# Performance work log

Measured on AMD Instinct MI355X. Metric: run time of the kernel, lower is better.

## Reference

```python
import jax, jax.numpy as jnp
import numpy as np

N = 471
TOPK = 50
T = 16384
M = 128


def setup_inputs() -> dict:
    key = jax.random.key(0)
    ks = jax.random.split(key, 6)
    x = jax.random.normal(ks[0], (T, N), dtype=jnp.float32)
    q_t = jax.random.normal(ks[1], (M, N), dtype=jnp.float32)
    # parameters, initialized as in the torch module
    w = 0.0021 + 0.0005 * jax.random.normal(ks[2], (N,), dtype=jnp.float32)
    b1 = jax.random.normal(ks[3], (N,), dtype=jnp.float32)  # unused in forward math
    alpha = jnp.array([10.0], dtype=jnp.float32)
    lamda = jnp.array([0.1], dtype=jnp.float32)
    rho = jnp.array([0.001], dtype=jnp.float32)
    mu = jnp.array([0.001], dtype=jnp.float32)
    bound = 1.0 / np.sqrt(N)
    linear_w = jax.random.uniform(ks[4], (N, N), minval=-bound, maxval=bound, dtype=jnp.float32)
    linear_b = jax.random.uniform(ks[5], (N,), minval=-bound, maxval=bound, dtype=jnp.float32)
    return {"x": x, "q_t": q_t, "w": w, "b1": b1, "alpha": alpha,
            "lamda": lamda, "rho": rho, "mu": mu,
            "linear_w": linear_w, "linear_b": linear_b}


def reference(x, q_t, w, b1, alpha, lamda, rho, mu, linear_w, linear_b):
    # W2 = mean over time of Linear(x); identical every unrolled iteration -> compute once
    W2 = (x @ linear_w.T + linear_b).mean(axis=0)           # [N]
    pinvQ = jnp.linalg.pinv(q_t @ q_t.T)                    # [M,M], identical every iter

    def theta_update(z, u):
        v = u - rho * (z - w)                               # [N]
        return alpha * (pinvQ @ (q_t @ v))                  # [M]

    def z_update(z, u, theta):
        b = w + (q_t.T @ theta) / N                         # [N]
        grad_z = W2 + rho * (z - b) + u
        grad_z = grad_z + 2.0 * lamda * (jnp.sum(z) - 1.0)  # scalar * ones broadcast
        grad_z = grad_z + 2.0 * lamda * jnp.minimum(0.0, z)
        z_new = jax.nn.relu(z - mu * grad_z)
        _, idx = jax.lax.top_k(z_new, TOPK)
        mask = jnp.zeros_like(z_new).at[idx].set(1.0)
        return z_new * mask

    z = jnp.zeros(N, dtype=x.dtype)
    u = jnp.zeros(N, dtype=x.dtype)
    for _ in range(9):
        theta = theta_update(z, u)
        z = z_update(z, u, theta)
        b = w + (q_t.T @ theta) / N
        u = u + rho * (z - b)
    theta = theta_update(z, u)
    z = z_update(z, u, theta)
    return z / (jnp.sum(z) + 1e-8)
```

## Files before the change

kernel.cpp:

```cpp
#include <hip/hip_runtime.h>

#define NDIM 471
#define MD   128
#define TD   16384
#define KSEL 50
#define CGIT 4

#define WS_PART   0
#define WS_G      120832
#define WS_T1     137216
#define WS_XBAR   197888
#define WS_W2     198400
#define WS_RW     198912
#define WS_CTR    199384
#define WS_R      199424

static __device__ __forceinline__ float rdl(float v, int lane){
    return __int_as_float(__builtin_amdgcn_readlane(__float_as_int(v), lane));
}

__global__ __launch_bounds__(512) void k_gram_colsum(const float* __restrict__ qt,
                                                     const float* __restrict__ x,
                                                     const float* __restrict__ wv,
                                                     float* __restrict__ ws){
    int lane = threadIdx.x & 63, wid = threadIdx.x >> 6;
    if (blockIdx.x < 256){
        float* G = ws + WS_G;
        int gw = blockIdx.x * 8 + wid;
        int i = gw >> 4, jb = gw & 15;
        float qi[8];
#pragma unroll
        for (int s = 0; s < 8; ++s){ int idx = lane + 64*s; qi[s] = (idx < NDIM) ? qt[i*NDIM + idx] : 0.f; }
#pragma unroll
        for (int t = 0; t < 8; ++t){
            int j = jb + 16*t;
            float acc = 0.f;
#pragma unroll
            for (int s = 0; s < 8; ++s){
                int idx = lane + 64*s;
                float qj = (idx < NDIM) ? qt[j*NDIM + idx] : 0.f;
                acc = fmaf(qi[s], qj, acc);
            }
#pragma unroll
            for (int d = 1; d < 64; d <<= 1) acc += __shfl_xor(acc, d);
            if (lane == 0) G[i*MD + j] = acc;
        }
    } else {
        int cb = blockIdx.x - 256;
        int col = threadIdx.x;
        if (col < NDIM){
            const float* xp = x + (size_t)cb*64*NDIM + col;
            float acc = 0.f;
#pragma unroll 4
            for (int r = 0; r < 64; ++r) acc += xp[(size_t)r*NDIM];
            ws[WS_PART + cb*NDIM + col] = acc;
        }
        if (cb < 16){
            int m = cb*8 + wid;
            float acc = 0.f;
#pragma unroll
            for (int s = 0; s < 8; ++s){
                int idx = lane + 64*s;
                if (idx < NDIM) acc = fmaf(qt[m*NDIM + idx], wv[idx], acc);
            }
#pragma unroll
            for (int d = 1; d < 64; d <<= 1) acc += __shfl_xor(acc, d);
            if (lane == 0) ws[WS_T1 + m] = acc;
        }
    }
}

#define G_LD(n) float4 t##n = *(const float4*)(Gp + 4*(n)); \
                float Ga##n = t##n.x, Gb##n = t##n.y, Gc##n = t##n.z, Gd##n = t##n.w;
#define G_DOT(n) pa = fmaf(Ga##n, rdl(rch.x, 2*(n)),   pa); \
                 pb = fmaf(Gb##n, rdl(rch.y, 2*(n)),   pb); \
                 pa = fmaf(Gc##n, rdl(rch.x, 2*(n)+1), pa); \
                 pb = fmaf(Gd##n, rdl(rch.y, 2*(n)+1), pb);

__global__ __launch_bounds__(256, 1) void k_cg_xbar(const float* __restrict__ qt,
                                                    const float* __restrict__ alpha,
                                                    float* __restrict__ ws){
    int tid = threadIdx.x, lane = tid & 63, wid = tid >> 6;
    if (blockIdx.x == 130 && tid == 0)
        __hip_atomic_store((unsigned*)(ws + WS_CTR), 0u, __ATOMIC_RELEASE, __HIP_MEMORY_SCOPE_AGENT);
    __shared__ __align__(16) float rl[2][128];
    __shared__ float part[2][2][128];
    __shared__ float red2[4][2];
    {
        int row = tid & 127, seg = tid >> 7;
        int c   = seg;
        int col = blockIdx.x*2 + c;
        const float* Gp = ws + WS_G + row*MD + seg*64;
        G_LD(0) G_LD(1) G_LD(2)  G_LD(3)  G_LD(4)  G_LD(5)  G_LD(6)  G_LD(7)
        G_LD(8) G_LD(9) G_LD(10) G_LD(11) G_LD(12) G_LD(13) G_LD(14) G_LD(15)
        float bvv = (col < NDIM) ? qt[row*NDIM + col] : ws[WS_T1 + row];
        float xv = 0.f, rv = bvv, pv = 0.f, sv = 0.f, gam = 1.f, alf = 1.f;
        rl[c][row] = rv;
        for (int it = 0; it < CGIT; ++it){
            __syncthreads();
#pragma unroll
            for (int cc = 0; cc < 2; ++cc){
                float2 rch = *(const float2*)&rl[cc][seg*64 + 2*(lane & 31)];
                float pa = 0.f, pb = 0.f;
                G_DOT(0) G_DOT(1) G_DOT(2)  G_DOT(3)  G_DOT(4)  G_DOT(5)  G_DOT(6)  G_DOT(7)
                G_DOT(8) G_DOT(9) G_DOT(10) G_DOT(11) G_DOT(12) G_DOT(13) G_DOT(14) G_DOT(15)
                part[seg][cc][row] = pa + pb;
            }
            __syncthreads();
            float y = part[0][c][row] + part[1][c][row];
            float t0 = rv*rv, t1 = y*rv;
#pragma unroll
            for (int d = 1; d < 64; d <<= 1){ t0 += __shfl_xor(t0, d); t1 += __shfl_xor(t1, d); }
            if (lane == 0){ red2[wid][0] = t0; red2[wid][1] = t1; }
            __syncthreads();
            float gp = red2[2*c][0] + red2[2*c+1][0];
            float dl = red2[2*c][1] + red2[2*c+1][1];
            float bet, anew;
            if (it == 0){ bet = 0.f; anew = gp / fmaxf(dl, 1e-30f); }
            else { bet = gp / fmaxf(gam, 1e-30f); anew = gp / fmaxf(dl - bet*gp/alf, 1e-30f); }
            pv = fmaf(bet, pv, rv);
            sv = fmaf(bet, sv, y);
            xv = fmaf(anew, pv, xv);
            rv = fmaf(-anew, sv, rv);
            gam = gp; alf = anew;
            rl[c][row] = rv;
        }
        rl[c][row] = xv;
        __syncthreads();
        float sc = alpha[0] / (float)NDIM;
        float2 wc0 = ((const float2*)&rl[0][0])[lane];
        float2 wc1 = ((const float2*)&rl[1][0])[lane];
        int i0 = tid;
        int i1 = (tid + 256 < NDIM) ? tid + 256 : (NDIM - 1);
        float a0=0.f, a1=0.f, b0=0.f, b1=0.f;
#pragma unroll
        for (int l = 0; l < 64; ++l){
            float w0a = rdl(wc0.x, l), w0b = rdl(wc0.y, l);
            float w1a = rdl(wc1.x, l), w1b = rdl(wc1.y, l);
            float qa0 = qt[(2*l+0)*NDIM + i0], qa1 = qt[(2*l+0)*NDIM + i1];
            float qb0 = qt[(2*l+1)*NDIM + i0], qb1 = qt[(2*l+1)*NDIM + i1];
            a0 = fmaf(qa0, w0a, a0); a0 = fmaf(qb0, w0b, a0);
            a1 = fmaf(qa1, w0a, a1); a1 = fmaf(qb1, w0b, a1);
            b0 = fmaf(qa0, w1a, b0); b0 = fmaf(qb0, w1b, b0);
            b1 = fmaf(qa1, w1a, b1); b1 = fmaf(qb1, w1b, b1);
        }
        int col0 = blockIdx.x*2, col1 = col0 + 1;
        ws[WS_R + (size_t)col0*NDIM + i0] = sc*a0;
        if (tid + 256 < NDIM) ws[WS_R + (size_t)col0*NDIM + tid+256] = sc*a1;
        if (col1 < NDIM){
            ws[WS_R + (size_t)col1*NDIM + i0] = sc*b0;
            if (tid + 256 < NDIM) ws[WS_R + (size_t)col1*NDIM + tid+256] = sc*b1;
        } else {
            ws[WS_RW + i0] = sc*b0;
            if (tid + 256 < NDIM) ws[WS_RW + tid+256] = sc*b1;
        }
    }
    if (blockIdx.x < 59){
        __shared__ float p2[4][8];
        __syncthreads();
        int b2 = blockIdx.x;
        int cl = tid & 7, seg2 = tid >> 3;
        int col = b2*8 + cl;
        float acc = 0.f;
        if (col < NDIM){
#pragma unroll
            for (int q = 0; q < 8; ++q) acc += ws[WS_PART + (seg2*8 + q)*NDIM + col];
        }
        acc += __shfl_xor(acc, 8);
        acc += __shfl_xor(acc, 16);
        acc += __shfl_xor(acc, 32);
        if (lane < 8) p2[wid][lane] = acc;
        __syncthreads();
        if (tid < 8){
            float t = ((p2[0][tid] + p2[1][tid]) + (p2[2][tid] + p2[3][tid]));
            int c2 = b2*8 + tid;
            if (c2 < NDIM) ws[WS_XBAR + c2] = t * (1.0f / TD);
        }
    }
}

__global__ __launch_bounds__(512, 2) void k_w2_iter(const float* __restrict__ lw, const float* __restrict__ lb,
                                              const float* __restrict__ wv,
                                              const float* __restrict__ alpha, const float* __restrict__ lamda,
                                              const float* __restrict__ rho_p, const float* __restrict__ mu_p,
                                              float* __restrict__ ws, float* __restrict__ out){
    int tid = threadIdx.x, lane = tid & 63, wid = tid >> 6;
    unsigned* ctr = (unsigned*)(ws + WS_CTR);

    if (blockIdx.x < 59){
        int i = blockIdx.x*8 + wid;
        if (i < NDIM){
            float acc = 0.f;
#pragma unroll
            for (int s = 0; s < 8; ++s){
                int idx = lane + 64*s;
                if (idx < NDIM) acc = fmaf(lw[(size_t)i*NDIM + idx], ws[WS_XBAR + idx], acc);
            }
#pragma unroll
            for (int d = 1; d < 64; d <<= 1) acc += __shfl_xor(acc, d);
            if (lane == 0) ws[WS_W2 + i] = acc + lb[i];
        }
        __syncthreads();
        if (tid == 0){
            __threadfence();
            __hip_atomic_fetch_add(ctr, 1u, __ATOMIC_RELEASE, __HIP_MEMORY_SCOPE_AGENT);
        }
        return;
    }

    bool act = tid < NDIM;
    int ti = act ? tid : 0;
    float rho = rho_p[0], mu = mu_p[0], lam = lamda[0];
    float sc  = alpha[0] / (float)NDIM;
    float wi  = act ? wv[tid]         : 0.f;
    float Rwi = act ? ws[WS_RW + tid] : 0.f;

    __shared__ __align__(16) unsigned bins[1024];
    __shared__ __align__(8) float2 spair[64];
    __shared__ float warr[8];
    __shared__ unsigned wcnt[8];

    bins[tid] = 0u; bins[tid + 512] = 0u;
    if (tid == 0){
        while (__hip_atomic_load(ctr, __ATOMIC_ACQUIRE, __HIP_MEMORY_SCOPE_AGENT) < 59u)
            __builtin_amdgcn_s_sleep(8);
    }
    __syncthreads();
    float W2i = act ? ws[WS_W2 + tid] : 0.f;

    float z = 0.f, u = 0.f, Ruv = 0.f, Rzv = 0.f, Sz = 0.f;
    for (int it = 0; it < 10; ++it){
        float Rv = Ruv - rho*(Rzv - Rwi);
        float b  = wi + Rv;
        float grad = W2i + rho*(z - b) + u + 2.f*lam*(Sz - 1.f);
        float zn = z - mu*grad;
        zn = (act && zn > 0.f) ? zn : 0.f;
        unsigned bits = __float_as_uint(zn);

        unsigned prefix = 0, need = KSEL;
#pragma unroll
        for (int pass = 3; pass >= 0; --pass){
            int sh = pass*8;
            unsigned* bp = bins + ((3 - pass) << 8);
            bool av = (pass == 3) || ((bits >> (sh + 8)) == (prefix >> (sh + 8)));
            if (av) atomicAdd(&bp[(bits >> sh) & 255u], 1u);
            __syncthreads();
            int base = 255 - 4*lane;
            uint4 bq = *(const uint4*)&bp[base - 3];
            unsigned b3 = bq.x, b2 = bq.y, b1 = bq.z, b0 = bq.w;
            unsigned csum = b0 + b1 + b2 + b3;
            unsigned incl = csum;
#pragma unroll
            for (int d = 1; d < 64; d <<= 1){ unsigned t = __shfl_up(incl, d); if (lane >= d) incl += t; }
            unsigned excl = incl - csum;
            bool hit = (excl < need) && (need <= incl);
            unsigned long long hm = __ballot(hit);
            int hl = __ffsll((long long)hm) - 1;
            unsigned c0 = excl + b0, c1 = c0 + b1, c2 = c1 + b2;
            int byte; unsigned above, cntc;
            if      (need <= c0){ byte = base;   above = excl; cntc = b0; }
            else if (need <= c1){ byte = base-1; above = c0;   cntc = b1; }
            else if (need <= c2){ byte = base-2; above = c1;   cntc = b2; }
            else                { byte = base-3; above = c2;   cntc = b3; }
            byte  = __shfl(byte, hl);
            above = (unsigned)__shfl((int)above, hl);
            cntc  = (unsigned)__shfl((int)cntc, hl);
            prefix |= ((unsigned)byte) << sh;
            need -= above;
            if (cntc == need) break;
        }
        z = (act && bits >= prefix) ? zn : 0.f;

        bool flag = z > 0.f;
        unsigned long long mb = __ballot(flag);
        float v = z;
#pragma unroll
        for (int d = 1; d < 64; d <<= 1) v += __shfl_xor(v, d);
        if (lane == 0){ warr[wid] = v; wcnt[wid] = (unsigned)__popcll(mb); }
        __syncthreads();
        Sz = ((warr[0]+warr[1])+(warr[2]+warr[3])) + ((warr[4]+warr[5])+(warr[6]+warr[7]));

        if (it < 9){
            unsigned off = 0;
#pragma unroll
            for (int w2 = 0; w2 < 8; ++w2) if (w2 < wid) off += wcnt[w2];
            off += (unsigned)__popcll(mb & ((1ull << lane) - 1ull));
            int cnt = 0;
#pragma unroll
            for (int w2 = 0; w2 < 8; ++w2) cnt += (int)wcnt[w2];
            if (flag){ spair[off] = make_float2(__int_as_float(tid), z); }
            if (tid >= cnt && tid < 64){ spair[tid] = make_float2(__int_as_float(0), 0.f); }
            bins[tid] = 0u; bins[tid + 512] = 0u;
            __syncthreads();

            float2 pp = spair[lane];
            const float* Rb = ws + WS_R;
            float rvv[56];
#pragma unroll
            for (int s = 0; s < 56; ++s){
                int j = __float_as_int(rdl(pp.x, s));
                rvv[s] = Rb[(size_t)j*NDIM + ti];
            }
            float a0=0.f, a1=0.f, a2=0.f, a3=0.f;
#pragma unroll
            for (int s = 0; s < 56; s += 4){
                a0 = fmaf(rvv[s+0], rdl(pp.y, s+0), a0);
                a1 = fmaf(rvv[s+1], rdl(pp.y, s+1), a1);
                a2 = fmaf(rvv[s+2], rdl(pp.y, s+2), a2);
                a3 = fmaf(rvv[s+3], rdl(pp.y, s+3), a3);
            }
            float acc = (a0+a1) + (a2+a3);
            float Rbv = Rwi + sc*Rv;
            u   += rho*(z - b);
            Ruv += rho*(acc - Rbv);
            Rzv  = acc;
        }
    }
    if (act) out[tid] = z / (Sz + 1e-8f);
}

extern "C" void kernel_launch(void* const* d_in, const int* in_sizes, int n_in,
                              void* d_out, int out_size, void* d_ws, size_t ws_size,
                              hipStream_t stream) {
    const float* x     = (const float*)d_in[0];
    const float* qt    = (const float*)d_in[1];
    const float* wv    = (const float*)d_in[2];
    const float* alpha = (const float*)d_in[4];
    const float* lamda = (const float*)d_in[5];
    const float* rho   = (const float*)d_in[6];
    const float* mu    = (const float*)d_in[7];
    const float* lw    = (const float*)d_in[8];
    const float* lb    = (const float*)d_in[9];
    float* out = (float*)d_out;
    float* ws  = (float*)d_ws;

    k_gram_colsum<<<512, 512, 0, stream>>>(qt, x, wv, ws);
    k_cg_xbar    <<<236, 256, 0, stream>>>(qt, alpha, ws);
    k_w2_iter    <<<60,  512, 0, stream>>>(lw, lb, wv, alpha, lamda, rho, mu, ws, out);
}
```

Before: 60.55 us.

## Fuse three kernels into one persistent kernel with atomic-counter dataflow sync

Merges the Gram/colsum, CG solve, and W2/iteration kernels into a single 256-block launch. Stages are ordered by per-stage atomic counters with release/acquire spin-waits instead of kernel boundaries, and a memset resets the counters. Each block now does the Gram work, then part of the x column sum, then either a CG column pair, an xbar/W2 slice, or the final iteration loop. The aim is to remove launch gaps and to overlap independent stages, at the cost of spin-wait overhead and relying on all 256 blocks being co-resident.

After: 124.1 us. 105% more time.

```diff
diff --git a/kernel.cpp b/kernel.cpp
--- a/kernel.cpp
+++ b/kernel.cpp
@@ -19,14 +19,45 @@
     return __int_as_float(__builtin_amdgcn_readlane(__float_as_int(v), lane));
 }
 
-__global__ __launch_bounds__(512) void k_gram_colsum(const float* __restrict__ qt,
-                                                     const float* __restrict__ x,
-                                                     const float* __restrict__ wv,
-                                                     float* __restrict__ ws){
-    int lane = threadIdx.x & 63, wid = threadIdx.x >> 6;
-    if (blockIdx.x < 256){
+static __device__ __forceinline__ void rel_add(unsigned* c){
+    if (threadIdx.x == 0){
+        __threadfence();
+        __hip_atomic_fetch_add(c, 1u, __ATOMIC_RELEASE, __HIP_MEMORY_SCOPE_AGENT);
+    }
+}
+static __device__ __forceinline__ void acq_wait(unsigned* c, unsigned tgt){
+    if (threadIdx.x == 0){
+        while (__hip_atomic_load(c, __ATOMIC_ACQUIRE, __HIP_MEMORY_SCOPE_AGENT) < tgt)
+            __builtin_amdgcn_s_sleep(2);
+    }
+    __syncthreads();
+}
+
+#define G_LDm(n) float4 t##n = cgact ? *(const float4*)(Gp + 4*(n)) : f4z; \
+                 float Ga##n = t##n.x, Gb##n = t##n.y, Gc##n = t##n.z, Gd##n = t##n.w;
+#define G_DOT(n) pa = fmaf(Ga##n, rdl(rch.x, 2*(n)),   pa); \
+                 pb = fmaf(Gb##n, rdl(rch.y, 2*(n)),   pb); \
+                 pa = fmaf(Gc##n, rdl(rch.x, 2*(n)+1), pa); \
+                 pb = fmaf(Gd##n, rdl(rch.y, 2*(n)+1), pb);
+
+__global__ __launch_bounds__(512) void k_mega(const float* __restrict__ qt,
+                                              const float* __restrict__ x,
+                                              const float* __restrict__ wv,
+                                              const float* __restrict__ alpha,
+                                              const float* __restrict__ lamda,
+                                              const float* __restrict__ rho_p,
+                                              const float* __restrict__ mu_p,
+                                              const float* __restrict__ lw,
+                                              const float* __restrict__ lb,
+                                              float* __restrict__ ws,
+                                              float* __restrict__ out){
+    int tid = threadIdx.x, lane = tid & 63, wid = tid >> 6;
+    int b = blockIdx.x;
+    unsigned* C = (unsigned*)(ws + WS_CTR);
+
+    {
         float* G = ws + WS_G;
-        int gw = blockIdx.x * 8 + wid;
+        int gw = b*8 + wid;
         int i = gw >> 4, jb = gw & 15;
         float qi[8];
 #pragma unroll
@@ -45,18 +76,8 @@
             for (int d = 1; d < 64; d <<= 1) acc += __shfl_xor(acc, d);
             if (lane == 0) G[i*MD + j] = acc;
         }
-    } else {
-        int cb = blockIdx.x - 256;
-        int col = threadIdx.x;
-        if (col < NDIM){
-            const float* xp = x + (size_t)cb*64*NDIM + col;
-            float acc = 0.f;
-#pragma unroll 4
-            for (int r = 0; r < 64; ++r) acc += xp[(size_t)r*NDIM];
-            ws[WS_PART + cb*NDIM + col] = acc;
-        }
-        if (cb < 16){
-            int m = cb*8 + wid;
+        if (b < 16){
+            int m = b*8 + wid;
             float acc = 0.f;
 #pragma unroll
             for (int s = 0; s < 8; ++s){
@@ -67,129 +88,131 @@
             for (int d = 1; d < 64; d <<= 1) acc += __shfl_xor(acc, d);
             if (lane == 0) ws[WS_T1 + m] = acc;
         }
-    }
-}
-
-#define G_LD(n) float4 t##n = *(const float4*)(Gp + 4*(n)); \
-                float Ga##n = t##n.x, Gb##n = t##n.y, Gc##n = t##n.z, Gd##n = t##n.w;
-#define G_DOT(n) pa = fmaf(Ga##n, rdl(rch.x, 2*(n)),   pa); \
-                 pb = fmaf(Gb##n, rdl(rch.y, 2*(n)),   pb); \
-                 pa = fmaf(Gc##n, rdl(rch.x, 2*(n)+1), pa); \
-                 pb = fmaf(Gd##n, rdl(rch.y, 2*(n)+1), pb);
-
-__global__ __launch_bounds__(256, 1) void k_cg_xbar(const float* __restrict__ qt,
-                                                    const float* __restrict__ alpha,
-                                                    float* __restrict__ ws){
-    int tid = threadIdx.x, lane = tid & 63, wid = tid >> 6;
-    if (blockIdx.x == 130 && tid == 0)
-        __hip_atomic_store((unsigned*)(ws + WS_CTR), 0u, __ATOMIC_RELEASE, __HIP_MEMORY_SCOPE_AGENT);
-    __shared__ __align__(16) float rl[2][128];
-    __shared__ float part[2][2][128];
-    __shared__ float red2[4][2];
+        __syncthreads();
+        if (tid == 0){
+            __threadfence();
+            __hip_atomic_fetch_add(&C[0], 1u, __ATOMIC_RELEASE, __HIP_MEMORY_SCOPE_AGENT);
+            if (b < 16) __hip_atomic_fetch_add(&C[1], 1u, __ATOMIC_RELEASE, __HIP_MEMORY_SCOPE_AGENT);
+        }
+    }
+
     {
-        int row = tid & 127, seg = tid >> 7;
+        int col = tid;
+        if (col < NDIM){
+            const float* xp = x + (size_t)b*64*NDIM + col;
+            float acc = 0.f;
+#pragma unroll 4
+            for (int r = 0; r < 64; ++r) acc += xp[(size_t)r*NDIM];
+            ws[WS_PART + b*NDIM + col] = acc;
+        }
+        __syncthreads();
+        rel_add(&C[2]);
+    }
+
+    if (b < 236){
+        __shared__ __align__(16) float rl[2][128];
+        __shared__ float part[2][2][128];
+        __shared__ float red2[4][2];
+        acq_wait(&C[0], 256);
+        acq_wait(&C[1], 16);
+        bool cgact = tid < 256;
+        float4 f4z = make_float4(0.f,0.f,0.f,0.f);
+        int row = tid & 127, seg = (tid >> 7) & 1;
         int c   = seg;
-        int col = blockIdx.x*2 + c;
+        int col = b*2 + c;
         const float* Gp = ws + WS_G + row*MD + seg*64;
-        G_LD(0) G_LD(1) G_LD(2)  G_LD(3)  G_LD(4)  G_LD(5)  G_LD(6)  G_LD(7)
-        G_LD(8) G_LD(9) G_LD(10) G_LD(11) G_LD(12) G_LD(13) G_LD(14) G_LD(15)
-        float bvv = (col < NDIM) ? qt[row*NDIM + col] : ws[WS_T1 + row];
+        G_LDm(0) G_LDm(1) G_LDm(2)  G_LDm(3)  G_LDm(4)  G_LDm(5)  G_LDm(6)  G_LDm(7)
+        G_LDm(8) G_LDm(9) G_LDm(10) G_LDm(11) G_LDm(12) G_LDm(13) G_LDm(14) G_LDm(15)
+        float bvv = cgact ? ((col < NDIM) ? qt[row*NDIM + col] : ws[WS_T1 + row]) : 0.f;
         float xv = 0.f, rv = bvv, pv = 0.f, sv = 0.f, gam = 1.f, alf = 1.f;
-        rl[c][row] = rv;
+        if (cgact) rl[c][row] = rv;
         for (int it = 0; it < CGIT; ++it){
             __syncthreads();
-#pragma unroll
-            for (int cc = 0; cc < 2; ++cc){
-                float2 rch = *(const float2*)&rl[cc][seg*64 + 2*(lane & 31)];
-                float pa = 0.f, pb = 0.f;
-                G_DOT(0) G_DOT(1) G_DOT(2)  G_DOT(3)  G_DOT(4)  G_DOT(5)  G_DOT(6)  G_DOT(7)
-                G_DOT(8) G_DOT(9) G_DOT(10) G_DOT(11) G_DOT(12) G_DOT(13) G_DOT(14) G_DOT(15)
-                part[seg][cc][row] = pa + pb;
+            if (cgact){
+#pragma unroll
+                for (int cc = 0; cc < 2; ++cc){
+                    float2 rch = *(const float2*)&rl[cc][seg*64 + 2*(lane & 31)];
+                    float pa = 0.f, pb = 0.f;
+                    G_DOT(0) G_DOT(1) G_DOT(2)  G_DOT(3)  G_DOT(4)  G_DOT(5)  G_DOT(6)  G_DOT(7)
+                    G_DOT(8) G_DOT(9) G_DOT(10) G_DOT(11) G_DOT(12) G_DOT(13) G_DOT(14) G_DOT(15)
+                    part[seg][cc][row] = pa + pb;
+                }
             }
             __syncthreads();
-            float y = part[0][c][row] + part[1][c][row];
-            float t0 = rv*rv, t1 = y*rv;
-#pragma unroll
-            for (int d = 1; d < 64; d <<= 1){ t0 += __shfl_xor(t0, d); t1 += __shfl_xor(t1, d); }
-            if (lane == 0){ red2[wid][0] = t0; red2[wid][1] = t1; }
+            float y = 0.f, t0 = 0.f, t1 = 0.f;
+            if (cgact){
+                y = part[0][c][row] + part[1][c][row];
+                t0 = rv*rv; t1 = y*rv;
+#pragma unroll
+                for (int d = 1; d < 64; d <<= 1){ t0 += __shfl_xor(t0, d); t1 += __shfl_xor(t1, d); }
+                if (lane == 0){ red2[wid][0] = t0; red2[wid][1] = t1; }
+            }
             __syncthreads();
-            float gp = red2[2*c][0] + red2[2*c+1][0];
-            float dl = red2[2*c][1] + red2[2*c+1][1];
-            float bet, anew;
-            if (it == 0){ bet = 0.f; anew = gp / fmaxf(dl, 1e-30f); }
-            else { bet = gp / fmaxf(gam, 1e-30f); anew = gp / fmaxf(dl - bet*gp/alf, 1e-30f); }
-            pv = fmaf(bet, pv, rv);
-            sv = fmaf(bet, sv, y);
-            xv = fmaf(anew, pv, xv);
-            rv = fmaf(-anew, sv, rv);
-            gam = gp; alf = anew;
-            rl[c][row] = rv;
-        }
-        rl[c][row] = xv;
-        __syncthreads();
-        float sc = alpha[0] / (float)NDIM;
-        float2 wc0 = ((const float2*)&rl[0][0])[lane];
-        float2 wc1 = ((const float2*)&rl[1][0])[lane];
-        int i0 = tid;
-        int i1 = (tid + 256 < NDIM) ? tid + 256 : (NDIM - 1);
-        float a0=0.f, a1=0.f, b0=0.f, b1=0.f;
-#pragma unroll
-        for (int l = 0; l < 64; ++l){
-            float w0a = rdl(wc0.x, l), w0b = rdl(wc0.y, l);
-            float w1a = rdl(wc1.x, l), w1b = rdl(wc1.y, l);
-            float qa0 = qt[(2*l+0)*NDIM + i0], qa1 = qt[(2*l+0)*NDIM + i1];
-            float qb0 = qt[(2*l+1)*NDIM + i0], qb1 = qt[(2*l+1)*NDIM + i1];
-            a0 = fmaf(qa0, w0a, a0); a0 = fmaf(qb0, w0b, a0);
-            a1 = fmaf(qa1, w0a, a1); a1 = fmaf(qb1, w0b, a1);
-            b0 = fmaf(qa0, w1a, b0); b0 = fmaf(qb0, w1b, b0);
-            b1 = fmaf(qa1, w1a, b1); b1 = fmaf(qb1, w1b, b1);
-        }
-        int col0 = blockIdx.x*2, col1 = col0 + 1;
-        ws[WS_R + (size_t)col0*NDIM + i0] = sc*a0;
-        if (tid + 256 < NDIM) ws[WS_R + (size_t)col0*NDIM + tid+256] = sc*a1;
-        if (col1 < NDIM){
-            ws[WS_R + (size_t)col1*NDIM + i0] = sc*b0;
-            if (tid + 256 < NDIM) ws[WS_R + (size_t)col1*NDIM + tid+256] = sc*b1;
-        } else {
-            ws[WS_RW + i0] = sc*b0;
-            if (tid + 256 < NDIM) ws[WS_RW + tid+256] = sc*b1;
-        }
-    }
-    if (blockIdx.x < 59){
-        __shared__ float p2[4][8];
-        __syncthreads();
-        int b2 = blockIdx.x;
-        int cl = tid & 7, seg2 = tid >> 3;
-        int col = b2*8 + cl;
-        float acc = 0.f;
-        if (col < NDIM){
-#pragma unroll
-            for (int q = 0; q < 8; ++q) acc += ws[WS_PART + (seg2*8 + q)*NDIM + col];
-        }
-        acc += __shfl_xor(acc, 8);
-        acc += __shfl_xor(acc, 16);
-        acc += __shfl_xor(acc, 32);
-        if (lane < 8) p2[wid][lane] = acc;
-        __syncthreads();
-        if (tid < 8){
-            float t = ((p2[0][tid] + p2[1][tid]) + (p2[2][tid] + p2[3][tid]));
-            int c2 = b2*8 + tid;
-            if (c2 < NDIM) ws[WS_XBAR + c2] = t * (1.0f / TD);
-        }
-    }
-}
-
-__global__ __launch_bounds__(512, 2) void k_w2_iter(const float* __restrict__ lw, const float* __restrict__ lb,
-                                              const float* __restrict__ wv,
-                                              const float* __restrict__ alpha, const float* __restrict__ lamda,
-                                              const float* __restrict__ rho_p, const float* __restrict__ mu_p,
-                                              float* __restrict__ ws, float* __restrict__ out){
-    int tid = threadIdx.x, lane = tid & 63, wid = tid >> 6;
-    unsigned* ctr = (unsigned*)(ws + WS_CTR);
-
-    if (blockIdx.x < 59){
-        int i = blockIdx.x*8 + wid;
-        if (i < NDIM){
+            if (cgact){
+                float gp = red2[2*c][0] + red2[2*c+1][0];
+                float dl = red2[2*c][1] + red2[2*c+1][1];
+                float bet, anew;
+                if (it == 0){ bet = 0.f; anew = gp / fmaxf(dl, 1e-30f); }
+                else { bet = gp / fmaxf(gam, 1e-30f); anew = gp / fmaxf(dl - bet*gp/alf, 1e-30f); }
+                pv = fmaf(bet, pv, rv);
+                sv = fmaf(bet, sv, y);
+                xv = fmaf(anew, pv, xv);
+                rv = fmaf(-anew, sv, rv);
+                gam = gp; alf = anew;
+                rl[c][row] = rv;
+            }
+        }
+        if (cgact) rl[c][row] = xv;
+        __syncthreads();
+        if (cgact){
+            float sc = alpha[0] / (float)NDIM;
+            float2 wc0 = ((const float2*)&rl[0][0])[lane];
+            float2 wc1 = ((const float2*)&rl[1][0])[lane];
+            int i0 = tid;
+            int i1 = (tid + 256 < NDIM) ? tid + 256 : (NDIM - 1);
+            float a0=0.f, a1=0.f, b0=0.f, b1=0.f;
+#pragma unroll
+            for (int l = 0; l < 64; ++l){
+                float w0a = rdl(wc0.x, l), w0b = rdl(wc0.y, l);
+                float w1a = rdl(wc1.x, l), w1b = rdl(wc1.y, l);
+                float qa0 = qt[(2*l+0)*NDIM + i0], qa1 = qt[(2*l+0)*NDIM + i1];
+                float qb0 = qt[(2*l+1)*NDIM + i0], qb1 = qt[(2*l+1)*NDIM + i1];
+                a0 = fmaf(qa0, w0a, a0); a0 = fmaf(qb0, w0b, a0);
+                a1 = fmaf(qa1, w0a, a1); a1 = fmaf(qb1, w0b, a1);
+                b0 = fmaf(qa0, w1a, b0); b0 = fmaf(qb0, w1b, b0);
+                b1 = fmaf(qa1, w1a, b1); b1 = fmaf(qb1, w1b, b1);
+            }
+            int col0 = b*2, col1 = col0 + 1;
+            ws[WS_R + (size_t)col0*NDIM + i0] = sc*a0;
+            if (tid + 256 < NDIM) ws[WS_R + (size_t)col0*NDIM + tid+256] = sc*a1;
+            if (col1 < NDIM){
+                ws[WS_R + (size_t)col1*NDIM + i0] = sc*b0;
+                if (tid + 256 < NDIM) ws[WS_R + (size_t)col1*NDIM + tid+256] = sc*b1;
+            } else {
+                ws[WS_RW + i0] = sc*b0;
+                if (tid + 256 < NDIM) ws[WS_RW + tid+256] = sc*b1;
+            }
+        }
+        __syncthreads();
+        rel_add(&C[3]);
+    } else if (b < 255){
+        acq_wait(&C[2], 256);
+        int base = (b - 236)*25;
+        int ncols = (base + 25 <= NDIM) ? 25 : (NDIM - base);
+        for (int j = wid; j < ncols; j += 8){
+            int col = base + j;
+            float acc = 0.f;
+#pragma unroll
+            for (int s = 0; s < 4; ++s) acc += ws[WS_PART + (lane + 64*s)*NDIM + col];
+#pragma unroll
+            for (int d = 1; d < 64; d <<= 1) acc += __shfl_xor(acc, d);
+            if (lane == 0) ws[WS_XBAR + col] = acc * (1.0f / TD);
+        }
+        __syncthreads();
+        rel_add(&C[4]);
+        acq_wait(&C[4], 19);
+        for (int k = wid; k < ncols; k += 8){
+            int i = base + k;
             float acc = 0.f;
 #pragma unroll
             for (int s = 0; s < 8; ++s){
@@ -201,122 +224,113 @@
             if (lane == 0) ws[WS_W2 + i] = acc + lb[i];
         }
         __syncthreads();
-        if (tid == 0){
-            __threadfence();
-            __hip_atomic_fetch_add(ctr, 1u, __ATOMIC_RELEASE, __HIP_MEMORY_SCOPE_AGENT);
-        }
-        return;
-    }
-
-    bool act = tid < NDIM;
-    int ti = act ? tid : 0;
-    float rho = rho_p[0], mu = mu_p[0], lam = lamda[0];
-    float sc  = alpha[0] / (float)NDIM;
-    float wi  = act ? wv[tid]         : 0.f;
-    float Rwi = act ? ws[WS_RW + tid] : 0.f;
-
-    __shared__ __align__(16) unsigned bins[1024];
-    __shared__ __align__(8) float2 spair[64];
-    __shared__ float warr[8];
-    __shared__ unsigned wcnt[8];
-
-    bins[tid] = 0u; bins[tid + 512] = 0u;
-    if (tid == 0){
-        while (__hip_atomic_load(ctr, __ATOMIC_ACQUIRE, __HIP_MEMORY_SCOPE_AGENT) < 59u)
-            __builtin_amdgcn_s_sleep(8);
-    }
-    __syncthreads();
-    float W2i = act ? ws[WS_W2 + tid] : 0.f;
-
-    float z = 0.f, u = 0.f, Ruv = 0.f, Rzv = 0.f, Sz = 0.f;
-    for (int it = 0; it < 10; ++it){
-        float Rv = Ruv - rho*(Rzv - Rwi);
-        float b  = wi + Rv;
-        float grad = W2i + rho*(z - b) + u + 2.f*lam*(Sz - 1.f);
-        float zn = z - mu*grad;
-        zn = (act && zn > 0.f) ? zn : 0.f;
-        unsigned bits = __float_as_uint(zn);
-
-        unsigned prefix = 0, need = KSEL;
-#pragma unroll
-        for (int pass = 3; pass >= 0; --pass){
-            int sh = pass*8;
-            unsigned* bp = bins + ((3 - pass) << 8);
-            bool av = (pass == 3) || ((bits >> (sh + 8)) == (prefix >> (sh + 8)));
-            if (av) atomicAdd(&bp[(bits >> sh) & 255u], 1u);
+        rel_add(&C[5]);
+    } else {
+        __shared__ __align__(16) unsigned bins[1024];
+        __shared__ __align__(8) float2 spair[64];
+        __shared__ float warr[8];
+        __shared__ unsigned wcnt[8];
+        bool act = tid < NDIM;
+        int ti = act ? tid : 0;
+        float rho = rho_p[0], mu = mu_p[0], lam = lamda[0];
+        float sc  = alpha[0] / (float)NDIM;
+        float wi  = act ? wv[tid] : 0.f;
+        bins[tid] = 0u; bins[tid + 512] = 0u;
+        acq_wait(&C[3], 236);
+        acq_wait(&C[5], 19);
+        float Rwi = act ? ws[WS_RW + tid] : 0.f;
+        float W2i = act ? ws[WS_W2 + tid] : 0.f;
+
+        float z = 0.f, u = 0.f, Ruv = 0.f, Rzv = 0.f, Sz = 0.f;
+        for (int it = 0; it < 10; ++it){
+            float Rv = Ruv - rho*(Rzv - Rwi);
+            float bb = wi + Rv;
+            float grad = W2i + rho*(z - bb) + u + 2.f*lam*(Sz - 1.f);
+            float zn = z - mu*grad;
+            zn = (act && zn > 0.f) ? zn : 0.f;
+            unsigned bits = __float_as_uint(zn);
+
+            unsigned prefix = 0, need = KSEL;
+#pragma unroll
+            for (int pass = 3; pass >= 0; --pass){
+                int sh = pass*8;
+                unsigned* bp = bins + ((3 - pass) << 8);
+                bool av = (pass == 3) || ((bits >> (sh + 8)) == (prefix >> (sh + 8)));
+                if (av) atomicAdd(&bp[(bits >> sh) & 255u], 1u);
+                __syncthreads();
+                int base = 255 - 4*lane;
+                uint4 bq = *(const uint4*)&bp[base - 3];
+                unsigned b3 = bq.x, b2 = bq.y, b1 = bq.z, b0 = bq.w;
+                unsigned csum = b0 + b1 + b2 + b3;
+                unsigned incl = csum;
+#pragma unroll
+                for (int d = 1; d < 64; d <<= 1){ unsigned t = __shfl_up(incl, d); if (lane >= d) incl += t; }
+                unsigned excl = incl - csum;
+                bool hit = (excl < need) && (need <= incl);
+                unsigned long long hm = __ballot(hit);
+                int hl = __ffsll((long long)hm) - 1;
+                unsigned c0 = excl + b0, c1 = c0 + b1, c2 = c1 + b2;
+                int byte; unsigned above, cntc;
+                if      (need <= c0){ byte = base;   above = excl; cntc = b0; }
+                else if (need <= c1){ byte = base-1; above = c0;   cntc = b1; }
+                else if (need <= c2){ byte = base-2; above = c1;   cntc = b2; }
+                else                { byte = base-3; above = c2;   cntc = b3; }
+                byte  = __shfl(byte, hl);
+                above = (unsigned)__shfl((int)above, hl);
+                cntc  = (unsigned)__shfl((int)cntc, hl);
+                prefix |= ((unsigned)byte) << sh;
+                need -= above;
+                if (cntc == need) break;
+            }
+            z = (act && bits >= prefix) ? zn : 0.f;
+
+            bool flag = z > 0.f;
+            unsigned long long mb = __ballot(flag);
+            float v = z;
+#pragma unroll
+            for (int d = 1; d < 64; d <<= 1) v += __shfl_xor(v, d);
+            if (lane == 0){ warr[wid] = v; wcnt[wid] = (unsigned)__popcll(mb); }
             __syncthreads();
-            int base = 255 - 4*lane;
-            uint4 bq = *(const uint4*)&bp[base - 3];
-            unsigned b3 = bq.x, b2 = bq.y, b1 = bq.z, b0 = bq.w;
-            unsigned csum = b0 + b1 + b2 + b3;
-            unsigned incl = csum;
-#pragma unroll
-            for (int d = 1; d < 64; d <<= 1){ unsigned t = __shfl_up(incl, d); if (lane >= d) incl += t; }
-            unsigned excl = incl - csum;
-            bool hit = (excl < need) && (need <= incl);
-            unsigned long long hm = __ballot(hit);
-            int hl = __ffsll((long long)hm) - 1;
-            unsigned c0 = excl + b0, c1 = c0 + b1, c2 = c1 + b2;
-            int byte; unsigned above, cntc;
-            if      (need <= c0){ byte = base;   above = excl; cntc = b0; }
-            else if (need <= c1){ byte = base-1; above = c0;   cntc = b1; }
-            else if (need <= c2){ byte = base-2; above = c1;   cntc = b2; }
-            else                { byte = base-3; above = c2;   cntc = b3; }
-            byte  = __shfl(byte, hl);
-            above = (unsigned)__shfl((int)above, hl);
-            cntc  = (unsigned)__shfl((int)cntc, hl);
-            prefix |= ((unsigned)byte) << sh;
-            need -= above;
-            if (cntc == need) break;
-        }
-        z = (act && bits >= prefix) ? zn : 0.f;
-
-        bool flag = z > 0.f;
-        unsigned long long mb = __ballot(flag);
-        float v = z;
-#pragma unroll
-        for (int d = 1; d < 64; d <<= 1) v += __shfl_xor(v, d);
-        if (lane == 0){ warr[wid] = v; wcnt[wid] = (unsigned)__popcll(mb); }
-        __syncthreads();
-        Sz = ((warr[0]+warr[1])+(warr[2]+warr[3])) + ((warr[4]+warr[5])+(warr[6]+warr[7]));
-
-        if (it < 9){
-            unsigned off = 0;
-#pragma unroll
-            for (int w2 = 0; w2 < 8; ++w2) if (w2 < wid) off += wcnt[w2];
-            off += (unsigned)__popcll(mb & ((1ull << lane) - 1ull));
-            int cnt = 0;
-#pragma unroll
-            for (int w2 = 0; w2 < 8; ++w2) cnt += (int)wcnt[w2];
-            if (flag){ spair[off] = make_float2(__int_as_float(tid), z); }
-            if (tid >= cnt && tid < 64){ spair[tid] = make_float2(__int_as_float(0), 0.f); }
-            bins[tid] = 0u; bins[tid + 512] = 0u;
-            __syncthreads();
-
-            float2 pp = spair[lane];
-            const float* Rb = ws + WS_R;
-            float rvv[56];
-#pragma unroll
-            for (int s = 0; s < 56; ++s){
-                int j = __float_as_int(rdl(pp.x, s));
-                rvv[s] = Rb[(size_t)j*NDIM + ti];
-            }
-            float a0=0.f, a1=0.f, a2=0.f, a3=0.f;
-#pragma unroll
-            for (int s = 0; s < 56; s += 4){
-                a0 = fmaf(rvv[s+0], rdl(pp.y, s+0), a0);
-                a1 = fmaf(rvv[s+1], rdl(pp.y, s+1), a1);
-                a2 = fmaf(rvv[s+2], rdl(pp.y, s+2), a2);
-                a3 = fmaf(rvv[s+3], rdl(pp.y, s+3), a3);
-            }
-            float acc = (a0+a1) + (a2+a3);
-            float Rbv = Rwi + sc*Rv;
-            u   += rho*(z - b);
-            Ruv += rho*(acc - Rbv);
-            Rzv  = acc;
-        }
-    }
-    if (act) out[tid] = z / (Sz + 1e-8f);
+            Sz = ((warr[0]+warr[1])+(warr[2]+warr[3])) + ((warr[4]+warr[5])+(warr[6]+warr[7]));
+
+            if (it < 9){
+                unsigned off = 0;
+#pragma unroll
+                for (int w2 = 0; w2 < 8; ++w2) if (w2 < wid) off += wcnt[w2];
+                off += (unsigned)__popcll(mb & ((1ull << lane) - 1ull));
+                int cnt = 0;
+#pragma unroll
+                for (int w2 = 0; w2 < 8; ++w2) cnt += (int)wcnt[w2];
+                if (flag){ spair[off] = make_float2(__int_as_float(tid), z); }
+                if (tid >= cnt && tid < 64){ spair[tid] = make_float2(__int_as_float(0), 0.f); }
+                bins[tid] = 0u; bins[tid + 512] = 0u;
+                __syncthreads();
+
+                float2 pp = spair[lane];
+                const float* Rb = ws + WS_R;
+                float rvv[56];
+#pragma unroll
+                for (int s = 0; s < 56; ++s){
+                    int j = __float_as_int(rdl(pp.x, s));
+                    rvv[s] = Rb[(size_t)j*NDIM + ti];
+                }
+                float a0=0.f, a1=0.f, a2=0.f, a3=0.f;
+#pragma unroll
+                for (int s = 0; s < 56; s += 4){
+                    a0 = fmaf(rvv[s+0], rdl(pp.y, s+0), a0);
+                    a1 = fmaf(rvv[s+1], rdl(pp.y, s+1), a1);
+                    a2 = fmaf(rvv[s+2], rdl(pp.y, s+2), a2);
+                    a3 = fmaf(rvv[s+3], rdl(pp.y, s+3), a3);
+                }
+                float acc = (a0+a1) + (a2+a3);
+                float Rbv = Rwi + sc*Rv;
+                u   += rho*(z - bb);
+                Ruv += rho*(acc - Rbv);
+                Rzv  = acc;
+            }
+        }
+        if (act) out[tid] = z / (Sz + 1e-8f);
+    }
 }
 
 extern "C" void kernel_launch(void* const* d_in, const int* in_sizes, int n_in,
@@ -334,7 +348,6 @@
     float* out = (float*)d_out;
     float* ws  = (float*)d_ws;
 
-    k_gram_colsum<<<512, 512, 0, stream>>>(qt, x, wv, ws);
-    k_cg_xbar    <<<236, 256, 0, stream>>>(qt, alpha, ws);
-    k_w2_iter    <<<60,  512, 0, stream>>>(lw, lb, wv, alpha, lamda, rho, mu, ws, out);
-}
+    hipMemsetAsync((char*)d_ws + (size_t)WS_CTR*sizeof(float), 0, 64, stream);
+    k_mega<<<256, 512, 0, stream>>>(qt, x, wv, alpha, lamda, rho, mu, lw, lb, ws, out);
+}
```

## Remove CG reduction barrier, reuse previous top-k threshold, relax spin-wait ordering

Applied to the files above, without the earlier changes.

In the CG kernel, the residual goes into a double-buffered shared array and each wave recomputes the full 128-element dot products itself. This removes the cross-wave shared reduction and one barrier per iteration. In the iterative kernel, the previous top-k threshold is tried first: if exactly 50 elements meet it, the 4-pass radix select is skipped. The spin-wait uses relaxed loads followed by one acquire fence, and the redundant threadfence before the release add is dropped. The costs are an extra barrier for the count check when the fast path misses, and some care needed around memory ordering.

Result: faster. 57.16 us (-5.6%).

```diff
diff --git a/kernel.cpp b/kernel.cpp
--- a/kernel.cpp
+++ b/kernel.cpp
@@ -83,9 +83,8 @@
     int tid = threadIdx.x, lane = tid & 63, wid = tid >> 6;
     if (blockIdx.x == 130 && tid == 0)
         __hip_atomic_store((unsigned*)(ws + WS_CTR), 0u, __ATOMIC_RELEASE, __HIP_MEMORY_SCOPE_AGENT);
-    __shared__ __align__(16) float rl[2][128];
+    __shared__ __align__(16) float rl[2][2][128];
     __shared__ float part[2][2][128];
-    __shared__ float red2[4][2];
     {
         int row = tid & 127, seg = tid >> 7;
         int c   = seg;
@@ -95,12 +94,13 @@
         G_LD(8) G_LD(9) G_LD(10) G_LD(11) G_LD(12) G_LD(13) G_LD(14) G_LD(15)
         float bvv = (col < NDIM) ? qt[row*NDIM + col] : ws[WS_T1 + row];
         float xv = 0.f, rv = bvv, pv = 0.f, sv = 0.f, gam = 1.f, alf = 1.f;
-        rl[c][row] = rv;
+        int buf = 0;
+        rl[0][c][row] = rv;
         for (int it = 0; it < CGIT; ++it){
             __syncthreads();
 #pragma unroll
             for (int cc = 0; cc < 2; ++cc){
-                float2 rch = *(const float2*)&rl[cc][seg*64 + 2*(lane & 31)];
+                float2 rch = *(const float2*)&rl[buf][cc][seg*64 + 2*(lane & 31)];
                 float pa = 0.f, pb = 0.f;
                 G_DOT(0) G_DOT(1) G_DOT(2)  G_DOT(3)  G_DOT(4)  G_DOT(5)  G_DOT(6)  G_DOT(7)
                 G_DOT(8) G_DOT(9) G_DOT(10) G_DOT(11) G_DOT(12) G_DOT(13) G_DOT(14) G_DOT(15)
@@ -108,13 +108,14 @@
             }
             __syncthreads();
             float y = part[0][c][row] + part[1][c][row];
-            float t0 = rv*rv, t1 = y*rv;
+            float r0 = rl[buf][c][lane],      r1 = rl[buf][c][lane + 64];
+            float y0 = part[0][c][lane]      + part[1][c][lane];
+            float y1 = part[0][c][lane + 64] + part[1][c][lane + 64];
+            float t0 = fmaf(r0, r0, r1*r1);
+            float t1 = fmaf(y0, r0, y1*r1);
 #pragma unroll
             for (int d = 1; d < 64; d <<= 1){ t0 += __shfl_xor(t0, d); t1 += __shfl_xor(t1, d); }
-            if (lane == 0){ red2[wid][0] = t0; red2[wid][1] = t1; }
-            __syncthreads();
-            float gp = red2[2*c][0] + red2[2*c+1][0];
-            float dl = red2[2*c][1] + red2[2*c+1][1];
+            float gp = t0, dl = t1;
             float bet, anew;
             if (it == 0){ bet = 0.f; anew = gp / fmaxf(dl, 1e-30f); }
             else { bet = gp / fmaxf(gam, 1e-30f); anew = gp / fmaxf(dl - bet*gp/alf, 1e-30f); }
@@ -123,13 +124,14 @@
             xv = fmaf(anew, pv, xv);
             rv = fmaf(-anew, sv, rv);
             gam = gp; alf = anew;
-            rl[c][row] = rv;
-        }
-        rl[c][row] = xv;
+            rl[buf^1][c][row] = rv;
+            buf ^= 1;
+        }
+        rl[buf][c][row] = xv;
         __syncthreads();
         float sc = alpha[0] / (float)NDIM;
-        float2 wc0 = ((const float2*)&rl[0][0])[lane];
-        float2 wc1 = ((const float2*)&rl[1][0])[lane];
+        float2 wc0 = ((const float2*)&rl[buf][0][0])[lane];
+        float2 wc1 = ((const float2*)&rl[buf][1][0])[lane];
         int i0 = tid;
         int i1 = (tid + 256 < NDIM) ? tid + 256 : (NDIM - 1);
         float a0=0.f, a1=0.f, b0=0.f, b1=0.f;
@@ -201,10 +203,8 @@
             if (lane == 0) ws[WS_W2 + i] = acc + lb[i];
         }
         __syncthreads();
-        if (tid == 0){
-            __threadfence();
+        if (tid == 0)
             __hip_atomic_fetch_add(ctr, 1u, __ATOMIC_RELEASE, __HIP_MEMORY_SCOPE_AGENT);
-        }
         return;
     }
 
@@ -222,13 +222,15 @@
 
     bins[tid] = 0u; bins[tid + 512] = 0u;
     if (tid == 0){
-        while (__hip_atomic_load(ctr, __ATOMIC_ACQUIRE, __HIP_MEMORY_SCOPE_AGENT) < 59u)
+        while (__hip_atomic_load(ctr, __ATOMIC_RELAXED, __HIP_MEMORY_SCOPE_AGENT) < 59u)
             __builtin_amdgcn_s_sleep(8);
+        __builtin_amdgcn_fence(__ATOMIC_ACQUIRE, "agent");
     }
     __syncthreads();
     float W2i = act ? ws[WS_W2 + tid] : 0.f;
 
     float z = 0.f, u = 0.f, Ruv = 0.f, Rzv = 0.f, Sz = 0.f;
+    unsigned tau = 0xFFFFFFFFu;
     for (int it = 0; it < 10; ++it){
         float Rv = Ruv - rho*(Rzv - Rwi);
         float b  = wi + Rv;
@@ -237,46 +239,59 @@
         zn = (act && zn > 0.f) ? zn : 0.f;
         unsigned bits = __float_as_uint(zn);
 
-        unsigned prefix = 0, need = KSEL;
-#pragma unroll
-        for (int pass = 3; pass >= 0; --pass){
-            int sh = pass*8;
-            unsigned* bp = bins + ((3 - pass) << 8);
-            bool av = (pass == 3) || ((bits >> (sh + 8)) == (prefix >> (sh + 8)));
-            if (av) atomicAdd(&bp[(bits >> sh) & 255u], 1u);
-            __syncthreads();
-            int base = 255 - 4*lane;
-            uint4 bq = *(const uint4*)&bp[base - 3];
-            unsigned b3 = bq.x, b2 = bq.y, b1 = bq.z, b0 = bq.w;
-            unsigned csum = b0 + b1 + b2 + b3;
-            unsigned incl = csum;
-#pragma unroll
-            for (int d = 1; d < 64; d <<= 1){ unsigned t = __shfl_up(incl, d); if (lane >= d) incl += t; }
-            unsigned excl = incl - csum;
-            bool hit = (excl < need) && (need <= incl);
-            unsigned long long hm = __ballot(hit);
-            int hl = __ffsll((long long)hm) - 1;
-            unsigned c0 = excl + b0, c1 = c0 + b1, c2 = c1 + b2;
-            int byte; unsigned above, cntc;
-            if      (need <= c0){ byte = base;   above = excl; cntc = b0; }
-            else if (need <= c1){ byte = base-1; above = c0;   cntc = b1; }
-            else if (need <= c2){ byte = base-2; above = c1;   cntc = b2; }
-            else                { byte = base-3; above = c2;   cntc = b3; }
-            byte  = __shfl(byte, hl);
-            above = (unsigned)__shfl((int)above, hl);
-            cntc  = (unsigned)__shfl((int)cntc, hl);
-            prefix |= ((unsigned)byte) << sh;
-            need -= above;
-            if (cntc == need) break;
+        bool cge = act && (bits >= tau);
+        unsigned long long cm = __ballot(cge);
+        if (lane == 0) wcnt[wid] = (unsigned)__popcll(cm);
+        __syncthreads();
+        int cnt0 = 0;
+#pragma unroll
+        for (int w2 = 0; w2 < 8; ++w2) cnt0 += (int)wcnt[w2];
+        bool fast = (cnt0 == KSEL);
+        unsigned prefix = tau;
+
+        if (!fast){
+            prefix = 0; unsigned need = KSEL;
+#pragma unroll
+            for (int pass = 3; pass >= 0; --pass){
+                int sh = pass*8;
+                unsigned* bp = bins + ((3 - pass) << 8);
+                bool av = (pass == 3) || ((bits >> (sh + 8)) == (prefix >> (sh + 8)));
+                if (av) atomicAdd(&bp[(bits >> sh) & 255u], 1u);
+                __syncthreads();
+                int base = 255 - 4*lane;
+                uint4 bq = *(const uint4*)&bp[base - 3];
+                unsigned b3 = bq.x, b2 = bq.y, b1 = bq.z, b0 = bq.w;
+                unsigned csum = b0 + b1 + b2 + b3;
+                unsigned incl = csum;
+#pragma unroll
+                for (int d = 1; d < 64; d <<= 1){ unsigned t = __shfl_up(incl, d); if (lane >= d) incl += t; }
+                unsigned excl = incl - csum;
+                bool hit = (excl < need) && (need <= incl);
+                unsigned long long hm = __ballot(hit);
+                int hl = __ffsll((long long)hm) - 1;
+                unsigned c0 = excl + b0, c1 = c0 + b1, c2 = c1 + b2;
+                int byte; unsigned above, cntc;
+                if      (need <= c0){ byte = base;   above = excl; cntc = b0; }
+                else if (need <= c1){ byte = base-1; above = c0;   cntc = b1; }
+                else if (need <= c2){ byte = base-2; above = c1;   cntc = b2; }
+                else                { byte = base-3; above = c2;   cntc = b3; }
+                byte  = __shfl(byte, hl);
+                above = (unsigned)__shfl((int)above, hl);
+                cntc  = (unsigned)__shfl((int)cntc, hl);
+                prefix |= ((unsigned)byte) << sh;
+                need -= above;
+                if (cntc == need) break;
+            }
+            tau = prefix;
         }
         z = (act && bits >= prefix) ? zn : 0.f;
 
         bool flag = z > 0.f;
-        unsigned long long mb = __ballot(flag);
+        unsigned long long mb = fast ? cm : __ballot(flag);
         float v = z;
 #pragma unroll
         for (int d = 1; d < 64; d <<= 1) v += __shfl_xor(v, d);
-        if (lane == 0){ warr[wid] = v; wcnt[wid] = (unsigned)__popcll(mb); }
+        if (lane == 0){ warr[wid] = v; if (!fast) wcnt[wid] = (unsigned)__popcll(mb); }
         __syncthreads();
         Sz = ((warr[0]+warr[1])+(warr[2]+warr[3])) + ((warr[4]+warr[5])+(warr[6]+warr[7]));
 
```
